# Performance work log

Hardware: AMD Instinct MI355X
Metric: run time of the kernel (lower is better)

The kernel has to match this reference:

```python
import jax, jax.numpy as jnp
import numpy as np

SMOOTH = 1e-05
NUM_CLASSES = 2  # binary segmentation labels {0,1}


def setup_inputs() -> dict:
    key = jax.random.key(0)
    k1, k2 = jax.random.split(key)
    shape = (32, 1, 1024, 1024)
    input = jax.random.normal(k1, shape, dtype=jnp.float32)
    target = jax.random.randint(k2, shape, 0, NUM_CLASSES, dtype=jnp.int32)
    return {"input": input, "target": target}


def reference(input, target):
    # sigmoid probabilities, flattened
    p = jax.nn.sigmoid(input).reshape(-1)
    t_int = target.reshape(-1)
    t = t_int.astype(p.dtype)

    # class-frequency histogram (fixed length -> jit-compatible)
    class_frequencies = jnp.bincount(t_int, length=NUM_CLASSES)
    class_weights = 1.0 / (class_frequencies.astype(p.dtype) + SMOOTH) ** 2
    w = class_weights[t_int]  # gather per-pixel weight

    intersection = jnp.sum(w * p * t)
    denominator = jnp.sum(w * (p * p + t * t))
    dice_loss = 1.0 - (2.0 * intersection + SMOOTH) / (denominator + SMOOTH)
    return dice_loss
```

## Files before the change

### kernel.cpp

```cpp
#include <hip/hip_runtime.h>

#define SMOOTH 1e-5

__global__ __launch_bounds__(256) void balanced_loss_stage1(
    const float* __restrict__ in, const int* __restrict__ tg,
    long long n, double* __restrict__ ws)
{
    const long long nvec = n >> 2;
    float lc1 = 0.f, ls1 = 0.f, lq0 = 0.f, lq1 = 0.f;

    const long long tid    = (long long)blockIdx.x * blockDim.x + threadIdx.x;
    const long long stride = (long long)gridDim.x * blockDim.x;
    const float4* __restrict__ in4 = (const float4*)in;
    const int4*  __restrict__ tg4 = (const int4*)tg;

#define PROC(xv, tv)                                        \
    {                                                       \
        float e  = __expf(-(xv));                           \
        float p  = __fdividef(1.f, 1.f + e);                \
        float pp = p * p;                                   \
        float ft = (tv) ? 1.f : 0.f;                        \
        lc1 += ft;                                          \
        ls1 += ft * p;                                      \
        lq1 += ft * pp;                                     \
        lq0 += (1.f - ft) * pp;                             \
    }

    long long i = tid;
    for (; i + 3 * stride < nvec; i += 4 * stride) {
        float4 x0 = in4[i];
        float4 x1 = in4[i + stride];
        float4 x2 = in4[i + 2 * stride];
        float4 x3 = in4[i + 3 * stride];
        int4   t0 = tg4[i];
        int4   t1 = tg4[i + stride];
        int4   t2 = tg4[i + 2 * stride];
        int4   t3 = tg4[i + 3 * stride];
        PROC(x0.x, t0.x); PROC(x0.y, t0.y); PROC(x0.z, t0.z); PROC(x0.w, t0.w);
        PROC(x1.x, t1.x); PROC(x1.y, t1.y); PROC(x1.z, t1.z); PROC(x1.w, t1.w);
        PROC(x2.x, t2.x); PROC(x2.y, t2.y); PROC(x2.z, t2.z); PROC(x2.w, t2.w);
        PROC(x3.x, t3.x); PROC(x3.y, t3.y); PROC(x3.z, t3.z); PROC(x3.w, t3.w);
    }
    for (; i < nvec; i += stride) {
        float4 x = in4[i];
        int4   t = tg4[i];
        PROC(x.x, t.x); PROC(x.y, t.y); PROC(x.z, t.z); PROC(x.w, t.w);
    }

    const long long tail0 = nvec << 2;
    if (blockIdx.x == 0) {
        for (long long j = tail0 + threadIdx.x; j < n; j += blockDim.x) {
            float x = in[j];
            int   t = tg[j];
            PROC(x, t);
        }
    }
#undef PROC

    double dc1 = (double)lc1, ds1 = (double)ls1;
    double dq0 = (double)lq0, dq1 = (double)lq1;
    for (int off = 32; off > 0; off >>= 1) {
        dc1 += __shfl_down(dc1, off, 64);
        ds1 += __shfl_down(ds1, off, 64);
        dq0 += __shfl_down(dq0, off, 64);
        dq1 += __shfl_down(dq1, off, 64);
    }

    __shared__ double sm[4][4];
    const int wid  = threadIdx.x >> 6;
    const int lane = threadIdx.x & 63;
    if (lane == 0) {
        sm[wid][0] = dc1; sm[wid][1] = ds1;
        sm[wid][2] = dq0; sm[wid][3] = dq1;
    }
    __syncthreads();
    if (threadIdx.x == 0) {
        double a0 = 0, a1 = 0, a2 = 0, a3 = 0;
        for (int w = 0; w < 4; ++w) {
            a0 += sm[w][0]; a1 += sm[w][1];
            a2 += sm[w][2]; a3 += sm[w][3];
        }
        double* p = ws + (size_t)blockIdx.x * 4;
        p[0] = a0; p[1] = a1; p[2] = a2; p[3] = a3;
    }
}

__global__ __launch_bounds__(256) void balanced_loss_stage2(
    const double* __restrict__ ws, int nblocks,
    float* __restrict__ out, long long n)
{
    double c1 = 0, s1 = 0, q0 = 0, q1 = 0;
    for (int b = threadIdx.x; b < nblocks; b += blockDim.x) {
        const double* p = ws + (size_t)b * 4;
        c1 += p[0]; s1 += p[1]; q0 += p[2]; q1 += p[3];
    }
    for (int off = 32; off > 0; off >>= 1) {
        c1 += __shfl_down(c1, off, 64);
        s1 += __shfl_down(s1, off, 64);
        q0 += __shfl_down(q0, off, 64);
        q1 += __shfl_down(q1, off, 64);
    }
    __shared__ double sm[4][4];
    const int wid  = threadIdx.x >> 6;
    const int lane = threadIdx.x & 63;
    if (lane == 0) {
        sm[wid][0] = c1; sm[wid][1] = s1;
        sm[wid][2] = q0; sm[wid][3] = q1;
    }
    __syncthreads();
    if (threadIdx.x == 0) {
        double a0 = 0, a1 = 0, a2 = 0, a3 = 0;
        for (int w = 0; w < 4; ++w) {
            a0 += sm[w][0]; a1 += sm[w][1];
            a2 += sm[w][2]; a3 += sm[w][3];
        }
        double cc1 = a0;
        double cc0 = (double)n - cc1;
        double w0 = 1.0 / ((cc0 + SMOOTH) * (cc0 + SMOOTH));
        double w1 = 1.0 / ((cc1 + SMOOTH) * (cc1 + SMOOTH));
        double I  = w1 * a1;
        double D  = w0 * a2 + w1 * (a3 + cc1);
        out[0] = (float)(1.0 - (2.0 * I + SMOOTH) / (D + SMOOTH));
    }
}

extern "C" void kernel_launch(void* const* d_in, const int* in_sizes, int n_in,
                              void* d_out, int out_size, void* d_ws, size_t ws_size,
                              hipStream_t stream) {
    const float* in = (const float*)d_in[0];
    const int*   tg = (const int*)d_in[1];
    long long n = (long long)in_sizes[0];
    double* ws = (double*)d_ws;

    const int block = 256;
    const int grid  = 2048;

    balanced_loss_stage1<<<grid, block, 0, stream>>>(in, tg, n, ws);
    balanced_loss_stage2<<<1, block, 0, stream>>>(ws, grid, (float*)d_out, n);
}
```

Measured before the change: 52.23 us.

## Use nontemporal loads, rcp intrinsic, simplified accumulators and wider final reduction

The input stream is now read with nontemporal loads, and the loads are interleaved and fenced with a sched_barrier. The fast divide becomes a raw rcp intrinsic. The per-element accumulators are simplified to sum p^2 over all pixels, and q0 is derived in stage 2 as total minus class-1. Stage 2 runs with 1024 threads. Together these aim to cut ALU work and cache pollution in a bandwidth-bound reduction, at a small risk of cancellation error in q0 = qa - q1.

```diff
diff --git a/kernel.cpp b/kernel.cpp
--- a/kernel.cpp
+++ b/kernel.cpp
@@ -2,48 +2,56 @@
 
 #define SMOOTH 1e-5
 
-__global__ __launch_bounds__(256) void balanced_loss_stage1(
+typedef float f32x4 __attribute__((ext_vector_type(4)));
+typedef int   i32x4 __attribute__((ext_vector_type(4)));
+
+__device__ __forceinline__ f32x4 ldnt(const f32x4* p) {
+    return __builtin_nontemporal_load(p);
+}
+
+__global__ __launch_bounds__(256, 8) void balanced_loss_stage1(
     const float* __restrict__ in, const int* __restrict__ tg,
     long long n, double* __restrict__ ws)
 {
     const long long nvec = n >> 2;
-    float lc1 = 0.f, ls1 = 0.f, lq0 = 0.f, lq1 = 0.f;
+    float lc1 = 0.f, ls1 = 0.f, lqa = 0.f, lq1 = 0.f;
 
     const long long tid    = (long long)blockIdx.x * blockDim.x + threadIdx.x;
     const long long stride = (long long)gridDim.x * blockDim.x;
-    const float4* __restrict__ in4 = (const float4*)in;
-    const int4*  __restrict__ tg4 = (const int4*)tg;
+    const f32x4* __restrict__ in4 = (const f32x4*)in;
+    const i32x4* __restrict__ tg4 = (const i32x4*)tg;
 
 #define PROC(xv, tv)                                        \
     {                                                       \
         float e  = __expf(-(xv));                           \
-        float p  = __fdividef(1.f, 1.f + e);                \
+        float p  = __builtin_amdgcn_rcpf(1.f + e);          \
         float pp = p * p;                                   \
-        float ft = (tv) ? 1.f : 0.f;                        \
+        float ft = (float)(tv);             \
+        lqa += pp;                                          \
         lc1 += ft;                                          \
         ls1 += ft * p;                                      \
         lq1 += ft * pp;                                     \
-        lq0 += (1.f - ft) * pp;                             \
     }
 
     long long i = tid;
     for (; i + 3 * stride < nvec; i += 4 * stride) {
-        float4 x0 = in4[i];
-        float4 x1 = in4[i + stride];
-        float4 x2 = in4[i + 2 * stride];
-        float4 x3 = in4[i + 3 * stride];
-        int4   t0 = tg4[i];
-        int4   t1 = tg4[i + stride];
-        int4   t2 = tg4[i + 2 * stride];
-        int4   t3 = tg4[i + 3 * stride];
+        f32x4 x0 = ldnt(in4 + i);
+        i32x4 t0 = tg4[i];
+        f32x4 x1 = ldnt(in4 + i + stride);
+        i32x4 t1 = tg4[i + stride];
+        f32x4 x2 = ldnt(in4 + i + 2 * stride);
+        i32x4 t2 = tg4[i + 2 * stride];
+        f32x4 x3 = ldnt(in4 + i + 3 * stride);
+        i32x4 t3 = tg4[i + 3 * stride];
+        __builtin_amdgcn_sched_barrier(0);
         PROC(x0.x, t0.x); PROC(x0.y, t0.y); PROC(x0.z, t0.z); PROC(x0.w, t0.w);
         PROC(x1.x, t1.x); PROC(x1.y, t1.y); PROC(x1.z, t1.z); PROC(x1.w, t1.w);
         PROC(x2.x, t2.x); PROC(x2.y, t2.y); PROC(x2.z, t2.z); PROC(x2.w, t2.w);
         PROC(x3.x, t3.x); PROC(x3.y, t3.y); PROC(x3.z, t3.z); PROC(x3.w, t3.w);
     }
     for (; i < nvec; i += stride) {
-        float4 x = in4[i];
-        int4   t = tg4[i];
+        f32x4 x = ldnt(in4 + i);
+        i32x4 t = tg4[i];
         PROC(x.x, t.x); PROC(x.y, t.y); PROC(x.z, t.z); PROC(x.w, t.w);
     }
 
@@ -58,11 +66,11 @@
 #undef PROC
 
     double dc1 = (double)lc1, ds1 = (double)ls1;
-    double dq0 = (double)lq0, dq1 = (double)lq1;
+    double dqa = (double)lqa, dq1 = (double)lq1;
     for (int off = 32; off > 0; off >>= 1) {
         dc1 += __shfl_down(dc1, off, 64);
         ds1 += __shfl_down(ds1, off, 64);
-        dq0 += __shfl_down(dq0, off, 64);
+        dqa += __shfl_down(dqa, off, 64);
         dq1 += __shfl_down(dq1, off, 64);
     }
 
@@ -71,7 +79,7 @@
     const int lane = threadIdx.x & 63;
     if (lane == 0) {
         sm[wid][0] = dc1; sm[wid][1] = ds1;
-        sm[wid][2] = dq0; sm[wid][3] = dq1;
+        sm[wid][2] = dqa; sm[wid][3] = dq1;
     }
     __syncthreads();
     if (threadIdx.x == 0) {
@@ -85,32 +93,33 @@
     }
 }
 
-__global__ __launch_bounds__(256) void balanced_loss_stage2(
+__global__ __launch_bounds__(1024) void balanced_loss_stage2(
     const double* __restrict__ ws, int nblocks,
     float* __restrict__ out, long long n)
 {
-    double c1 = 0, s1 = 0, q0 = 0, q1 = 0;
+    double c1 = 0, s1 = 0, qa = 0, q1 = 0;
     for (int b = threadIdx.x; b < nblocks; b += blockDim.x) {
         const double* p = ws + (size_t)b * 4;
-        c1 += p[0]; s1 += p[1]; q0 += p[2]; q1 += p[3];
+        c1 += p[0]; s1 += p[1]; qa += p[2]; q1 += p[3];
     }
     for (int off = 32; off > 0; off >>= 1) {
         c1 += __shfl_down(c1, off, 64);
         s1 += __shfl_down(s1, off, 64);
-        q0 += __shfl_down(q0, off, 64);
+        qa += __shfl_down(qa, off, 64);
         q1 += __shfl_down(q1, off, 64);
     }
-    __shared__ double sm[4][4];
+    __shared__ double sm[16][4];
     const int wid  = threadIdx.x >> 6;
     const int lane = threadIdx.x & 63;
     if (lane == 0) {
         sm[wid][0] = c1; sm[wid][1] = s1;
-        sm[wid][2] = q0; sm[wid][3] = q1;
+        sm[wid][2] = qa; sm[wid][3] = q1;
     }
     __syncthreads();
     if (threadIdx.x == 0) {
         double a0 = 0, a1 = 0, a2 = 0, a3 = 0;
-        for (int w = 0; w < 4; ++w) {
+        const int nw = blockDim.x >> 6;
+        for (int w = 0; w < nw; ++w) {
             a0 += sm[w][0]; a1 += sm[w][1];
             a2 += sm[w][2]; a3 += sm[w][3];
         }
@@ -118,8 +127,9 @@
         double cc0 = (double)n - cc1;
         double w0 = 1.0 / ((cc0 + SMOOTH) * (cc0 + SMOOTH));
         double w1 = 1.0 / ((cc1 + SMOOTH) * (cc1 + SMOOTH));
+        double q0 = a2 - a3;
         double I  = w1 * a1;
-        double D  = w0 * a2 + w1 * (a3 + cc1);
+        double D  = w0 * q0 + w1 * (a3 + cc1);
         out[0] = (float)(1.0 - (2.0 * I + SMOOTH) / (D + SMOOTH));
     }
 }
@@ -136,5 +146,5 @@
     const int grid  = 2048;
 
     balanced_loss_stage1<<<grid, block, 0, stream>>>(in, tg, n, ws);
-    balanced_loss_stage2<<<1, block, 0, stream>>>(ws, grid, (float*)d_out, n);
+    balanced_loss_stage2<<<1, 1024, 0, stream>>>(ws, grid, (float*)d_out, n);
 }
```

After: 51.07 us. -2.2%, faster.
